# Kernel optimization log

Hardware: AMD Instinct MI355X
Metric: run time of the kernel (lower is better)

Reference implementation:

```python
import jax, jax.numpy as jnp
import numpy as np

BIG_NUM = 1000000000.0

def setup_inputs() -> dict:
    key0 = jax.random.key(0)
    k1, k2, k3, k4 = jax.random.split(key0, 4)
    B, T, D = 64, 4096, 512
    query = jax.random.normal(k1, (B, D), dtype=jnp.float32)
    key = jax.random.normal(k2, (B, T, D), dtype=jnp.float32)
    value = jax.random.normal(k3, (B, T, D), dtype=jnp.float32)
    mask = jax.random.randint(k4, (B, T), 0, 2, dtype=jnp.int32)
    return {"query": query, "key": key, "value": value, "mask": mask}

def reference(query, key, value, mask):
    # query: [B, D], key/value: [B, T, D], mask: [B, T] (1 = keep, 0 = mask)
    D = query.shape[1]
    scale = D ** 0.5
    # energy[b, t] = key[b, t, :] . query[b, :]
    energy = jnp.einsum('btd,bd->bt', key, query) / scale
    energy = energy + (mask.astype(jnp.float32) - 1.0) * BIG_NUM
    attn = jax.nn.softmax(energy, axis=-1)          # [B, T]
    context = jnp.einsum('bt,btd->bd', attn, value)  # [B, D]
    return (context, attn)
```

## Files before the change

### kernel.cpp

```cpp
#include <hip/hip_runtime.h>
#include <math.h>

#define B 64
#define T 4096
#define D 512
#define NCH 32
#define CHT (T / NCH)
#define WSTRIP 32
#define VBATCH 8

typedef __attribute__((address_space(1))) const void global_cv;
typedef __attribute__((address_space(3))) void lds_v;

__device__ __forceinline__ float wave_sum64(float v) {
#pragma unroll
    for (int off = 32; off; off >>= 1)
        v += __shfl_xor(v, off, 64);
    return v;
}

__device__ __forceinline__ void stage_row(const float* __restrict__ gsrc_row,
                                          float* lds_row, int lane) {
    __builtin_amdgcn_global_load_lds((global_cv*)(gsrc_row + lane * 4),
                                     (lds_v*)(lds_row), 16, 0, 0);
    __builtin_amdgcn_global_load_lds((global_cv*)(gsrc_row + 256 + lane * 4),
                                     (lds_v*)(lds_row + 256), 16, 0, 0);
}

__global__ __launch_bounds__(256) void energy_exp_kernel(const float* __restrict__ q,
                                                         const float* __restrict__ k,
                                                         const int* __restrict__ mask,
                                                         float* __restrict__ attn,
                                                         float* __restrict__ chunk_sums) {
    const float INV_SCALE = 0.04419417382415922f;

    __shared__ int sm_list[4][WSTRIP];
    __shared__ float sred[4];

    int blk = blockIdx.x;
    int b = blk >> 5;
    int ch = blk & 31;
    int wave = threadIdx.x >> 6;
    int lane = threadIdx.x & 63;

    const float* qb = q + b * D;
    float4 qa = *(const float4*)(qb + lane * 4);
    float4 qc = *(const float4*)(qb + 256 + lane * 4);

    int t0 = ch * CHT + wave * WSTRIP;
    const float* kbase = k + ((size_t)b * T + t0) * D;

    int mv = (lane < WSTRIP) ? mask[b * T + t0 + lane] : 0;
    unsigned int mbits = (unsigned int)__ballot(mv != 0);
    int cnt = __popc(mbits);
    if (lane < WSTRIP) {
        if (mv != 0) {
            int pre = __popc(mbits & ((1u << lane) - 1u));
            sm_list[wave][pre] = lane;
        } else {
            attn[(size_t)b * T + t0 + lane] = 0.0f;
        }
    }

    int r3 = ((lane >> 5) & 1) | (((lane >> 4) & 1) << 1) | (((lane >> 3) & 1) << 2);
    float gsum = 0.f;
    int ngrp = (cnt + 7) >> 3;

#pragma unroll 1
    for (int g = 0; g < ngrp; ++g) {
        float d8[8];
#pragma unroll
        for (int rr = 0; rr < 8; ++rr) {
            int slot = g * 8 + rr;
            int row = sm_list[wave][slot < cnt ? slot : 0];
            const float* kr = kbase + (size_t)row * D;
            float4 ka = *(const float4*)(kr + lane * 4);
            float4 kc = *(const float4*)(kr + 256 + lane * 4);
            d8[rr] = ka.x * qa.x + ka.y * qa.y + ka.z * qa.z + ka.w * qa.w
                   + kc.x * qc.x + kc.y * qc.y + kc.z * qc.z + kc.w * qc.w;
        }
        bool b5 = (lane & 32) != 0;
        float e[4];
#pragma unroll
        for (int i = 0; i < 4; ++i) {
            float u = b5 ? d8[2*i+1] : d8[2*i];
            float s = b5 ? d8[2*i]   : d8[2*i+1];
            e[i] = u + __shfl_xor(s, 32, 64);
        }
        bool b4 = (lane & 16) != 0;
        float f[2];
#pragma unroll
        for (int i = 0; i < 2; ++i) {
            float u = b4 ? e[2*i+1] : e[2*i];
            float s = b4 ? e[2*i]   : e[2*i+1];
            f[i] = u + __shfl_xor(s, 16, 64);
        }
        bool b3 = (lane & 8) != 0;
        float u = b3 ? f[1] : f[0];
        float s = b3 ? f[0] : f[1];
        float h = u + __shfl_xor(s, 8, 64);
        h += __shfl_xor(h, 4, 64);
        h += __shfl_xor(h, 2, 64);
        h += __shfl_xor(h, 1, 64);

        int slot = g * 8 + r3;
        float gval = 0.f;
        if (slot < cnt) {
            gval = __expf(h * INV_SCALE);
            if ((lane & 7) == 0) {
                int row = sm_list[wave][slot];
                attn[(size_t)b * T + t0 + row] = gval;
            }
        }
        gsum += gval;
    }

    float ws = wave_sum64(gsum) * 0.125f;
    if (lane == 0) sred[wave] = ws;
    __syncthreads();
    if (threadIdx.x == 0)
        chunk_sums[blk] = (sred[0] + sred[1]) + (sred[2] + sred[3]);
}

__global__ __launch_bounds__(256) void context_partial_kernel(float* __restrict__ attn,
                                                              const float* __restrict__ v,
                                                              const float* __restrict__ chunk_sums,
                                                              float* __restrict__ partial) {
    __shared__ __align__(16) float vbuf[2][VBATCH][D];
    __shared__ float sa_raw[CHT];
    __shared__ int   rows[CHT + VBATCH];
    __shared__ float avals[CHT + VBATCH];
    __shared__ int   scnt;

    int blk = blockIdx.x;
    int b = blk >> 5;
    int ch = blk & 31;
    int tid = threadIdx.x;
    int wave = tid >> 6;
    int lane = tid & 63;

    float cs = (lane < NCH) ? chunk_sums[b * NCH + lane] : 0.f;
    float denom = wave_sum64(cs);
    float inv = 1.0f / denom;

    if (tid < CHT) sa_raw[tid] = attn[(size_t)b * T + ch * CHT + tid];
    __syncthreads();

    if (wave == 0) {
        float a0 = sa_raw[lane];
        unsigned long long bl0 = __ballot(a0 != 0.0f);
        int c0 = __popcll(bl0);
        if (a0 != 0.0f) {
            int p = __popcll(bl0 & ((1ull << lane) - 1ull));
            rows[p] = lane; avals[p] = a0;
        }
        float a1 = sa_raw[64 + lane];
        unsigned long long bl1 = __ballot(a1 != 0.0f);
        int c1 = __popcll(bl1);
        if (a1 != 0.0f) {
            int p = c0 + __popcll(bl1 & ((1ull << lane) - 1ull));
            rows[p] = 64 + lane; avals[p] = a1;
        }
        int cnt = c0 + c1;
        if (lane < VBATCH) {
            int safe0 = (cnt > 0) ? rows[0] : 0;
            rows[cnt + lane] = safe0;
            avals[cnt + lane] = 0.0f;
        }
        if (lane == 0) scnt = cnt;
    }
    __syncthreads();

    int cnt = scnt;
    int nb = (cnt + VBATCH - 1) / VBATCH;
    const float* vchunk = v + ((size_t)b * T + ch * CHT) * D;

    if (nb > 0) {
        int s0 = wave * 2;
        stage_row(vchunk + (size_t)rows[s0] * D,     &vbuf[0][wave * 2][0],     lane);
        stage_row(vchunk + (size_t)rows[s0 + 1] * D, &vbuf[0][wave * 2 + 1][0], lane);
    }
    if (nb > 1) {
        int s0 = VBATCH + wave * 2;
        stage_row(vchunk + (size_t)rows[s0] * D,     &vbuf[1][wave * 2][0],     lane);
        stage_row(vchunk + (size_t)rows[s0 + 1] * D, &vbuf[1][wave * 2 + 1][0], lane);
    }

    float2 acc = {0.f, 0.f};
    int c0 = tid * 2;
#pragma unroll 1
    for (int i = 0; i < nb; ++i) {
        if (i + 1 < nb) asm volatile("s_waitcnt vmcnt(4)" ::: "memory");
        else            asm volatile("s_waitcnt vmcnt(0)" ::: "memory");
        __builtin_amdgcn_s_barrier();

        const float (*buf)[D] = vbuf[i & 1];
        int base = i * VBATCH;
#pragma unroll
        for (int r = 0; r < VBATCH; ++r) {
            float a = avals[base + r];
            float2 vv = *(const float2*)&buf[r][c0];
            acc.x += a * vv.x;
            acc.y += a * vv.y;
        }
        __builtin_amdgcn_s_barrier();

        if (i + 2 < nb) {
            int s0 = (i + 2) * VBATCH + wave * 2;
            stage_row(vchunk + (size_t)rows[s0] * D,     &vbuf[i & 1][wave * 2][0],     lane);
            stage_row(vchunk + (size_t)rows[s0 + 1] * D, &vbuf[i & 1][wave * 2 + 1][0], lane);
        }
    }

    acc.x *= inv; acc.y *= inv;
    *(float2*)(partial + (size_t)(b * NCH + ch) * D + c0) = acc;

    if (tid < CHT)
        attn[(size_t)b * T + ch * CHT + tid] = sa_raw[tid] * inv;
}

__global__ __launch_bounds__(256) void context_reduce_kernel(const float* __restrict__ partial,
                                                             float* __restrict__ ctx) {
    int b = blockIdx.x;
    int tid = threadIdx.x;
    int d0 = tid * 2;
    float2 acc = {0.f, 0.f};
#pragma unroll 8
    for (int j = 0; j < NCH; ++j) {
        float2 p = *(const float2*)(partial + (size_t)(b * NCH + j) * D + d0);
        acc.x += p.x;
        acc.y += p.y;
    }
    *(float2*)(ctx + (size_t)b * D + d0) = acc;
}

extern "C" void kernel_launch(void* const* d_in, const int* in_sizes, int n_in,
                              void* d_out, int out_size, void* d_ws, size_t ws_size,
                              hipStream_t stream) {
    const float* q    = (const float*)d_in[0];
    const float* k    = (const float*)d_in[1];
    const float* v    = (const float*)d_in[2];
    const int*   mask = (const int*)d_in[3];

    float* ctx  = (float*)d_out;
    float* attn = (float*)d_out + B * D;

    float* chunk_sums = (float*)d_ws;
    float* partial    = (float*)d_ws + 8192;

    energy_exp_kernel<<<B * NCH, 256, 0, stream>>>(q, k, mask, attn, chunk_sums);
    context_partial_kernel<<<B * NCH, 256, 0, stream>>>(attn, v, chunk_sums, partial);
    context_reduce_kernel<<<B, 256, 0, stream>>>(partial, ctx);
}
```

Baseline: 112.9 us.

## Stage key rows into LDS with double-buffered async loads in energy kernel

The energy kernel now gathers the unmasked key rows into a per-wave double-buffered LDS staging area with global_load_lds, prefetching two batches of four rows ahead, instead of loading eight rows directly into registers per group. The reduction tree is reshaped for four rows per group and the duplicate-count scaling factor is adjusted to match. The aim is to overlap key memory latency with the dot-product compute. The cost is 64KB of LDS per block, which may limit occupancy, plus extra LDS traffic and waitcnt synchronisation; no barrier is needed since each wave uses its own buffer.

```diff
diff --git a/kernel.cpp b/kernel.cpp
--- a/kernel.cpp
+++ b/kernel.cpp
@@ -7,6 +7,7 @@
 #define NCH 32
 #define CHT (T / NCH)
 #define WSTRIP 32
+#define KBATCH 4
 #define VBATCH 8
 
 typedef __attribute__((address_space(1))) const void global_cv;
@@ -34,7 +35,8 @@
                                                          float* __restrict__ chunk_sums) {
     const float INV_SCALE = 0.04419417382415922f;
 
-    __shared__ int sm_list[4][WSTRIP];
+    __shared__ __align__(16) float kbuf[2][4][KBATCH][D];
+    __shared__ int sm_list[4][WSTRIP + KBATCH];
     __shared__ float sred[4];
 
     int blk = blockIdx.x;
@@ -53,6 +55,7 @@
     int mv = (lane < WSTRIP) ? mask[b * T + t0 + lane] : 0;
     unsigned int mbits = (unsigned int)__ballot(mv != 0);
     int cnt = __popc(mbits);
+    int row0 = (cnt > 0) ? (__ffs(mbits) - 1) : 0;
     if (lane < WSTRIP) {
         if (mv != 0) {
             int pre = __popc(mbits & ((1u << lane) - 1u));
@@ -61,53 +64,69 @@
             attn[(size_t)b * T + t0 + lane] = 0.0f;
         }
     }
-
-    int r3 = ((lane >> 5) & 1) | (((lane >> 4) & 1) << 1) | (((lane >> 3) & 1) << 2);
+    if (lane < KBATCH) sm_list[wave][cnt + lane] = row0;
+
+    int ngrp = (cnt + KBATCH - 1) >> 2;
+
+    if (ngrp > 0) {
+#pragma unroll
+        for (int r = 0; r < KBATCH; ++r)
+            stage_row(kbase + (size_t)sm_list[wave][r] * D, &kbuf[0][wave][r][0], lane);
+    }
+    if (ngrp > 1) {
+#pragma unroll
+        for (int r = 0; r < KBATCH; ++r)
+            stage_row(kbase + (size_t)sm_list[wave][KBATCH + r] * D, &kbuf[1][wave][r][0], lane);
+    }
+
+    int r2 = ((lane >> 5) & 1) | (((lane >> 4) & 1) << 1);
     float gsum = 0.f;
-    int ngrp = (cnt + 7) >> 3;
 
 #pragma unroll 1
-    for (int g = 0; g < ngrp; ++g) {
-        float d8[8];
-#pragma unroll
-        for (int rr = 0; rr < 8; ++rr) {
-            int slot = g * 8 + rr;
-            int row = sm_list[wave][slot < cnt ? slot : 0];
-            const float* kr = kbase + (size_t)row * D;
-            float4 ka = *(const float4*)(kr + lane * 4);
-            float4 kc = *(const float4*)(kr + 256 + lane * 4);
-            d8[rr] = ka.x * qa.x + ka.y * qa.y + ka.z * qa.z + ka.w * qa.w
+    for (int i = 0; i < ngrp; ++i) {
+        if (i + 1 < ngrp) asm volatile("s_waitcnt vmcnt(8)" ::: "memory");
+        else              asm volatile("s_waitcnt vmcnt(0)" ::: "memory");
+
+        const float (*buf)[D] = kbuf[i & 1][wave];
+        float d4[KBATCH];
+#pragma unroll
+        for (int rr = 0; rr < KBATCH; ++rr) {
+            float4 ka = *(const float4*)&buf[rr][lane * 4];
+            float4 kc = *(const float4*)&buf[rr][256 + lane * 4];
+            d4[rr] = ka.x * qa.x + ka.y * qa.y + ka.z * qa.z + ka.w * qa.w
                    + kc.x * qc.x + kc.y * qc.y + kc.z * qc.z + kc.w * qc.w;
         }
+        asm volatile("s_waitcnt lgkmcnt(0)" ::: "memory");
+        if (i + 2 < ngrp) {
+            int s0 = (i + 2) * KBATCH;
+#pragma unroll
+            for (int r = 0; r < KBATCH; ++r)
+                stage_row(kbase + (size_t)sm_list[wave][s0 + r] * D,
+                          &kbuf[i & 1][wave][r][0], lane);
+        }
+
         bool b5 = (lane & 32) != 0;
-        float e[4];
-#pragma unroll
-        for (int i = 0; i < 4; ++i) {
-            float u = b5 ? d8[2*i+1] : d8[2*i];
-            float s = b5 ? d8[2*i]   : d8[2*i+1];
-            e[i] = u + __shfl_xor(s, 32, 64);
+        float e[2];
+#pragma unroll
+        for (int j = 0; j < 2; ++j) {
+            float u = b5 ? d4[2*j+1] : d4[2*j];
+            float s = b5 ? d4[2*j]   : d4[2*j+1];
+            e[j] = u + __shfl_xor(s, 32, 64);
         }
         bool b4 = (lane & 16) != 0;
-        float f[2];
-#pragma unroll
-        for (int i = 0; i < 2; ++i) {
-            float u = b4 ? e[2*i+1] : e[2*i];
-            float s = b4 ? e[2*i]   : e[2*i+1];
-            f[i] = u + __shfl_xor(s, 16, 64);
-        }
-        bool b3 = (lane & 8) != 0;
-        float u = b3 ? f[1] : f[0];
-        float s = b3 ? f[0] : f[1];
-        float h = u + __shfl_xor(s, 8, 64);
+        float u = b4 ? e[1] : e[0];
+        float s = b4 ? e[0] : e[1];
+        float h = u + __shfl_xor(s, 16, 64);
+        h += __shfl_xor(h, 8, 64);
         h += __shfl_xor(h, 4, 64);
         h += __shfl_xor(h, 2, 64);
         h += __shfl_xor(h, 1, 64);
 
-        int slot = g * 8 + r3;
+        int slot = i * KBATCH + r2;
         float gval = 0.f;
         if (slot < cnt) {
             gval = __expf(h * INV_SCALE);
-            if ((lane & 7) == 0) {
+            if ((lane & 15) == 0) {
                 int row = sm_list[wave][slot];
                 attn[(size_t)b * T + t0 + row] = gval;
             }
@@ -115,7 +134,7 @@
         gsum += gval;
     }
 
-    float ws = wave_sum64(gsum) * 0.125f;
+    float ws = wave_sum64(gsum) * 0.0625f;
     if (lane == 0) sred[wave] = ws;
     __syncthreads();
     if (threadIdx.x == 0)
```

Result: no change. 111.4 us (-1.4%).
